# Kernel tuning notes

Hardware: AMD Instinct MI355X
Metric: run time of the kernel (lower is better)

The kernel has to match this reference:

```python
import jax, jax.numpy as jnp
import numpy as np

N = 50000      # nodes
E = 1600000    # edges (before self loops)
D = 128        # feature dim (input == hidden == final)
L = 3          # num_layers
EPS = 1e-5     # BatchNorm1d eps
SLOPE = 0.2    # GATConv leaky_relu negative slope


def setup_inputs() -> dict:
    key = jax.random.key(0)
    ks = jax.random.split(key, 5)
    x = jax.random.normal(ks[0], (N, D), jnp.float32)
    edge_index = jax.random.randint(ks[1], (2, E), 0, N)
    W = jax.random.normal(ks[2], (L, D, D), jnp.float32) * 0.1
    a_src = jax.random.normal(ks[3], (L, D), jnp.float32) * 0.1
    a_dst = jax.random.normal(ks[4], (L, D), jnp.float32) * 0.1
    b = jnp.zeros((L, D), jnp.float32)
    return {"x": x, "edge_index": edge_index, "W": W,
            "a_src": a_src, "a_dst": a_dst, "b": b}


def _gat_forward(x, src, dst, W, a_src, a_dst, b):
    z = x
    for l in range(L):
        h = z @ W[l]                                   # [N, D]
        # per-edge attention logits: alpha_src[j] + alpha_dst[i]
        e = jax.nn.leaky_relu((h @ a_src[l])[src] + (h @ a_dst[l])[dst], SLOPE)
        # segment softmax over incoming edges of each destination node
        m = jax.lax.stop_gradient(jax.ops.segment_max(e, dst, num_segments=N))
        p = jnp.exp(e - m[dst])
        s = jax.ops.segment_sum(p, dst, num_segments=N)
        alpha = p / s[dst]                             # [E+N]
        # scatter-aggregate weighted source features, add conv bias
        z = jax.ops.segment_sum(alpha[:, None] * h[src], dst, num_segments=N) + b[l]
        # fresh BatchNorm1d (training mode, weight=1, bias=0, biased var) -> ReLU
        mu = jnp.mean(z, axis=0)
        var = jnp.var(z, axis=0)
        z = jax.nn.relu((z - mu) * jax.lax.rsqrt(var + EPS))
        # dropout(p=0.5): identity in deterministic/eval reference
    return z


def reference(x, edge_index, W, a_src, a_dst, b):
    loops = jnp.arange(N, dtype=edge_index.dtype)
    src = jnp.concatenate([edge_index[0], loops])      # GATConv add_self_loops=True
    dst = jnp.concatenate([edge_index[1], loops])
    return _gat_forward(x, src, dst, W, a_src, a_dst, b)
```

## Files before the change

### kernel.cpp

```cpp
#include <hip/hip_runtime.h>
#include <hip/hip_bf16.h>
#include <math.h>

#define N_NODES 50000
#define N_EDGES 1600000
#define DIM 128
#define EPS 1e-5f
#define SLOPE 0.2f

#define NBUCK 256
#define NPB 196
#define EPB 4096
#define NBLK_B ((N_EDGES + EPB - 1) / EPB)

typedef __attribute__((ext_vector_type(8))) short bf16x8;
typedef __attribute__((ext_vector_type(4))) float f32x4;

__device__ __forceinline__ float lrelu(float x) { return x > 0.f ? x : SLOPE * x; }

__device__ __forceinline__ unsigned short f2bf(float f) {
    unsigned u = __float_as_uint(f);
    unsigned r = (u + 0x7fffu + ((u >> 16) & 1u)) >> 16;
    return (unsigned short)r;
}

__device__ __forceinline__ float2 ldh2(const unsigned short* p) {
    unsigned u = *(const unsigned*)p;
    float2 r;
    r.x = __uint_as_float(u << 16);
    r.y = __uint_as_float(u & 0xffff0000u);
    return r;
}

__global__ void k_hist(const int* __restrict__ dst, int* __restrict__ bcnt) {
    __shared__ int h[NBUCK];
    int tid = threadIdx.x;
    h[tid] = 0;
    __syncthreads();
    int nq = N_EDGES / 4;
    for (int q = blockIdx.x * 256 + tid; q < nq; q += gridDim.x * 256) {
        int4 d = ((const int4*)dst)[q];
        atomicAdd(&h[d.x / NPB], 1);
        atomicAdd(&h[d.y / NPB], 1);
        atomicAdd(&h[d.z / NPB], 1);
        atomicAdd(&h[d.w / NPB], 1);
    }
    __syncthreads();
    if (h[tid]) atomicAdd(&bcnt[tid], h[tid]);
}

__global__ void k_bscan(const int* __restrict__ bcnt, int* __restrict__ bbase,
                        int* __restrict__ gtail) {
    __shared__ int s[NBUCK];
    int t = threadIdx.x;
    int v = bcnt[t];
    s[t] = v;
    __syncthreads();
    for (int off = 1; off < NBUCK; off <<= 1) {
        int x = s[t];
        int y = (t >= off) ? s[t - off] : 0;
        __syncthreads();
        s[t] = x + y;
        __syncthreads();
    }
    bbase[t] = s[t] - v;
    gtail[t] = s[t] - v;
    if (t == NBUCK - 1) bbase[NBUCK] = s[NBUCK - 1];
}

__global__ __launch_bounds__(256) void k_partB(const int* __restrict__ src,
                                               const int* __restrict__ dst,
                                               int* __restrict__ gtail,
                                               uint2* __restrict__ staged) {
    __shared__ int cnt[NBUCK];
    __shared__ int bas[NBUCK];
    int tid = threadIdx.x;
    cnt[tid] = 0;
    __syncthreads();
    int e0 = blockIdx.x * EPB;
#pragma unroll 4
    for (int i = 0; i < EPB / 256; ++i) {
        int e = e0 + i * 256 + tid;
        if (e < N_EDGES) atomicAdd(&cnt[dst[e] / NPB], 1);
    }
    __syncthreads();
    {
        int c = cnt[tid];
        bas[tid] = c ? atomicAdd(&gtail[tid], c) : 0;
    }
    __syncthreads();
    cnt[tid] = 0;
    __syncthreads();
#pragma unroll 4
    for (int i = 0; i < EPB / 256; ++i) {
        int e = e0 + i * 256 + tid;
        if (e < N_EDGES) {
            int d = dst[e], s = src[e];
            int b = d / NPB;
            int off = atomicAdd(&cnt[b], 1);
            staged[bas[b] + off] = make_uint2((unsigned)s, (unsigned)d);
        }
    }
}

__global__ __launch_bounds__(256) void k_partC(const uint2* __restrict__ staged,
                                               const int* __restrict__ bbase,
                                               int* __restrict__ row_ptr,
                                               int* __restrict__ col_src) {
    __shared__ int cnt[NBUCK];
    __shared__ int loc[NBUCK];
    __shared__ int s[NBUCK];
    int b = blockIdx.x, tid = threadIdx.x;
    int d0 = b * NPB;
    int d1 = d0 + NPB;
    if (d1 > N_NODES) d1 = N_NODES;
    int nn = d1 - d0;
    int s0 = bbase[b], s1 = bbase[b + 1];

    cnt[tid] = 0;
    __syncthreads();
    for (int e = s0 + tid; e < s1; e += 256) {
        int d = (int)staged[e].y;
        atomicAdd(&cnt[d - d0], 1);
    }
    __syncthreads();
    {
        int v = cnt[tid];
        s[tid] = v;
        __syncthreads();
        for (int off = 1; off < NBUCK; off <<= 1) {
            int x = s[tid];
            int y = (tid >= off) ? s[tid - off] : 0;
            __syncthreads();
            s[tid] = x + y;
            __syncthreads();
        }
        loc[tid] = s[tid] - v;
    }
    if (tid < nn) row_ptr[d0 + tid] = s0 + loc[tid];
    if (b == 0 && tid == 0) row_ptr[N_NODES] = N_EDGES;
    cnt[tid] = 0;
    __syncthreads();
    for (int e = s0 + tid; e < s1; e += 256) {
        uint2 sd = staged[e];
        int d = (int)sd.y;
        int pos = s0 + loc[d - d0] + atomicAdd(&cnt[d - d0], 1);
        col_src[pos] = (int)sd.x;
    }
}

__global__ void k_prepW(const float* __restrict__ W, unsigned short* __restrict__ Wt) {
    int idx = blockIdx.x * 256 + threadIdx.x;
    int l = idx >> 14;
    int k = (idx >> 7) & 127;
    int c = idx & 127;
    Wt[l * 16384 + c * 128 + k] = f2bf(W[l * 16384 + k * 128 + c]);
}

__global__ __launch_bounds__(256) void k_gemm_mfma(const float* __restrict__ Z,
                                                   const unsigned short* __restrict__ Wt,
                                                   unsigned short* __restrict__ Hb,
                                                   const float* __restrict__ mu,
                                                   const float* __restrict__ rs,
                                                   const float* __restrict__ a_src,
                                                   const float* __restrict__ a_dst,
                                                   float* __restrict__ as_,
                                                   float* __restrict__ ad_) {
    __shared__ unsigned short Bs[128 * 128];
    int tid = threadIdx.x;
    int lane = tid & 63, wave = tid >> 6;

    {
        int c = tid >> 1, kh = tid & 1;
        const unsigned short* gsrc = &Wt[c * 128 + kh * 64];
#pragma unroll
        for (int ch = 0; ch < 8; ++ch) {
            int byte_off = (c * 256 + kh * 128 + ch * 16) ^ ((c & 7) << 4);
            *(int4*)((char*)Bs + byte_off) = *(const int4*)(gsrc + ch * 8);
        }
    }

    int r0 = blockIdx.x * 128 + wave * 32;
    bf16x8 afr[2][4];
#pragma unroll
    for (int rt = 0; rt < 2; ++rt) {
        int row = r0 + rt * 16 + (lane & 15);
        const float* zrow = &Z[(size_t)row * 128];
#pragma unroll
        for (int ks = 0; ks < 4; ++ks) {
            int k = ks * 32 + (lane >> 4) * 8;
            bf16x8 fr = (bf16x8){0, 0, 0, 0, 0, 0, 0, 0};
            if (row < N_NODES) {
                float4 a = *(const float4*)&zrow[k];
                float4 b = *(const float4*)&zrow[k + 4];
                if (mu) {
                    float4 m0 = *(const float4*)&mu[k];
                    float4 m1 = *(const float4*)&mu[k + 4];
                    float4 r0v = *(const float4*)&rs[k];
                    float4 r1v = *(const float4*)&rs[k + 4];
                    a.x = fmaxf((a.x - m0.x) * r0v.x, 0.f);
                    a.y = fmaxf((a.y - m0.y) * r0v.y, 0.f);
                    a.z = fmaxf((a.z - m0.z) * r0v.z, 0.f);
                    a.w = fmaxf((a.w - m0.w) * r0v.w, 0.f);
                    b.x = fmaxf((b.x - m1.x) * r1v.x, 0.f);
                    b.y = fmaxf((b.y - m1.y) * r1v.y, 0.f);
                    b.z = fmaxf((b.z - m1.z) * r1v.z, 0.f);
                    b.w = fmaxf((b.w - m1.w) * r1v.w, 0.f);
                }
                fr[0] = (short)f2bf(a.x); fr[1] = (short)f2bf(a.y);
                fr[2] = (short)f2bf(a.z); fr[3] = (short)f2bf(a.w);
                fr[4] = (short)f2bf(b.x); fr[5] = (short)f2bf(b.y);
                fr[6] = (short)f2bf(b.z); fr[7] = (short)f2bf(b.w);
            }
            afr[rt][ks] = fr;
        }
    }

    float asv[8], adv[8];
#pragma unroll
    for (int ct = 0; ct < 8; ++ct) {
        int c = ct * 16 + (lane & 15);
        asv[ct] = a_src[c];
        adv[ct] = a_dst[c];
    }
    __syncthreads();

    f32x4 acc[2][8];
#pragma unroll
    for (int rt = 0; rt < 2; ++rt)
#pragma unroll
        for (int ct = 0; ct < 8; ++ct) acc[rt][ct] = (f32x4){0.f, 0.f, 0.f, 0.f};

#pragma unroll
    for (int ct = 0; ct < 8; ++ct) {
        int c = ct * 16 + (lane & 15);
#pragma unroll
        for (int ks = 0; ks < 4; ++ks) {
            int k = ks * 32 + (lane >> 4) * 8;
            int byte_off = (c * 256 + k * 2) ^ ((c & 7) << 4);
            bf16x8 bfr = *(const bf16x8*)((char*)Bs + byte_off);
            acc[0][ct] = __builtin_amdgcn_mfma_f32_16x16x32_bf16(afr[0][ks], bfr, acc[0][ct], 0, 0, 0);
            acc[1][ct] = __builtin_amdgcn_mfma_f32_16x16x32_bf16(afr[1][ks], bfr, acc[1][ct], 0, 0, 0);
        }
    }

#pragma unroll
    for (int rt = 0; rt < 2; ++rt) {
#pragma unroll
        for (int ct = 0; ct < 8; ++ct) {
            int c = ct * 16 + (lane & 15);
#pragma unroll
            for (int j = 0; j < 4; ++j) {
                int row = r0 + rt * 16 + (lane >> 4) * 4 + j;
                if (row < N_NODES) Hb[(size_t)row * 128 + c] = f2bf(acc[rt][ct][j]);
            }
        }
#pragma unroll
        for (int j = 0; j < 4; ++j) {
            float ps = 0.f, pd = 0.f;
#pragma unroll
            for (int ct = 0; ct < 8; ++ct) {
                float v = acc[rt][ct][j];
                ps += v * asv[ct];
                pd += v * adv[ct];
            }
#pragma unroll
            for (int off = 8; off; off >>= 1) {
                ps += __shfl_xor(ps, off);
                pd += __shfl_xor(pd, off);
            }
            int row = r0 + rt * 16 + (lane >> 4) * 4 + j;
            if ((lane & 15) == 0 && row < N_NODES) {
                as_[row] = ps;
                ad_[row] = pd;
            }
        }
    }
}

__global__ void k_aggregate(const int* __restrict__ row_ptr, const int* __restrict__ col_src,
                            const unsigned short* __restrict__ Hb,
                            const float* __restrict__ as_, const float* __restrict__ ad_,
                            const float* __restrict__ bias, float* __restrict__ Zout,
                            float* __restrict__ ebuf) {
    int node = blockIdx.x * 4 + (threadIdx.x >> 6);
    int lane = threadIdx.x & 63;
    if (node >= N_NODES) return;

    int start = row_ptr[node], end = row_ptr[node + 1];
    int deg = end - start;
    float ad_i = ad_[node];
    float eself = lrelu(as_[node] + ad_i);
    float m = eself;
    float2 acc;
    float2 hi = ldh2(&Hb[(size_t)node * 128 + lane * 2]);

    if (deg <= 128) {
        int s0 = 0, s1 = 0;
        float e0 = -INFINITY, e1 = -INFINITY;
        if (start + lane < end) {
            s0 = col_src[start + lane];
            e0 = lrelu(as_[s0] + ad_i);
            m = fmaxf(m, e0);
        }
        if (start + 64 + lane < end) {
            s1 = col_src[start + 64 + lane];
            e1 = lrelu(as_[s1] + ad_i);
            m = fmaxf(m, e1);
        }
#pragma unroll
        for (int off = 32; off; off >>= 1) m = fmaxf(m, __shfl_xor(m, off));
        float w0 = __expf(e0 - m);
        float w1 = __expf(e1 - m);
        float p = w0 + w1;
#pragma unroll
        for (int off = 32; off; off >>= 1) p += __shfl_xor(p, off);
        float pself = __expf(eself - m);
        float inv_s = 1.f / (p + pself);
        w0 *= inv_s;
        w1 *= inv_s;
        float wself = pself * inv_s;
        acc.x = wself * hi.x;
        acc.y = wself * hi.y;

        int jmax = deg < 64 ? deg : 64;
        int j = 0;
        for (; j + 8 <= jmax; j += 8) {
            float w[8]; int sv[8];
#pragma unroll
            for (int q = 0; q < 8; ++q) {
                w[q] = __shfl(w0, j + q);
                sv[q] = __shfl(s0, j + q);
            }
            float2 h[8];
#pragma unroll
            for (int q = 0; q < 8; ++q) h[q] = ldh2(&Hb[(size_t)sv[q] * 128 + lane * 2]);
#pragma unroll
            for (int q = 0; q < 8; ++q) {
                acc.x += w[q] * h[q].x;
                acc.y += w[q] * h[q].y;
            }
        }
        for (; j < jmax; ++j) {
            float w = __shfl(w0, j);
            int sv = __shfl(s0, j);
            float2 hs = ldh2(&Hb[(size_t)sv * 128 + lane * 2]);
            acc.x += w * hs.x;
            acc.y += w * hs.y;
        }
        for (j = 64; j < deg; ++j) {
            float w = __shfl(w1, j - 64);
            int sv = __shfl(s1, j - 64);
            float2 hs = ldh2(&Hb[(size_t)sv * 128 + lane * 2]);
            acc.x += w * hs.x;
            acc.y += w * hs.y;
        }
    } else {
        for (int j = start + lane; j < end; j += 64) {
            int sj = col_src[j];
            float e = lrelu(as_[sj] + ad_i);
            ebuf[j] = e;
            m = fmaxf(m, e);
        }
#pragma unroll
        for (int off = 32; off; off >>= 1) m = fmaxf(m, __shfl_xor(m, off));
        float p = 0.f;
        for (int j = start + lane; j < end; j += 64) p += __expf(ebuf[j] - m);
#pragma unroll
        for (int off = 32; off; off >>= 1) p += __shfl_xor(p, off);
        float pself = __expf(eself - m);
        float inv_s = 1.f / (p + pself);
        float wself = pself * inv_s;
        acc.x = wself * hi.x;
        acc.y = wself * hi.y;
        for (int j = start; j < end; ++j) {
            int sv = col_src[j];
            float w = __expf(ebuf[j] - m) * inv_s;
            float2 hs = ldh2(&Hb[(size_t)sv * 128 + lane * 2]);
            acc.x += w * hs.x;
            acc.y += w * hs.y;
        }
    }

    float2 bv = *(const float2*)&bias[lane * 2];
    float2 o;
    o.x = acc.x + bv.x;
    o.y = acc.y + bv.y;
    *(float2*)&Zout[(size_t)node * 128 + lane * 2] = o;
}

__global__ void k_bnstats(const float* __restrict__ Z, float* __restrict__ part) {
    int c = threadIdx.x;
    float s = 0.f, sq = 0.f;
    for (int i = blockIdx.x; i < N_NODES; i += gridDim.x) {
        float v = Z[(size_t)i * 128 + c];
        s += v;
        sq += v * v;
    }
    part[blockIdx.x * 256 + c] = s;
    part[blockIdx.x * 256 + 128 + c] = sq;
}

__global__ void k_bnfinal(const float* __restrict__ part, float* __restrict__ mu,
                          float* __restrict__ rs) {
    int c = threadIdx.x;
    float s = 0.f, sq = 0.f;
    for (int b = 0; b < 512; ++b) {
        s += part[b * 256 + c];
        sq += part[b * 256 + 128 + c];
    }
    float m = s / (float)N_NODES;
    float var = sq / (float)N_NODES - m * m;
    mu[c] = m;
    rs[c] = rsqrtf(var + EPS);
}

__global__ void k_bnapply(const float* __restrict__ Zin, const float* __restrict__ mu,
                          const float* __restrict__ rs, float* __restrict__ Zout) {
    int idx = blockIdx.x * blockDim.x + threadIdx.x;
    if (idx >= N_NODES * 32) return;
    int c4 = idx & 31;
    float4 v = ((const float4*)Zin)[idx];
    float4 m4 = ((const float4*)mu)[c4];
    float4 r4 = ((const float4*)rs)[c4];
    v.x = fmaxf((v.x - m4.x) * r4.x, 0.f);
    v.y = fmaxf((v.y - m4.y) * r4.y, 0.f);
    v.z = fmaxf((v.z - m4.z) * r4.z, 0.f);
    v.w = fmaxf((v.w - m4.w) * r4.w, 0.f);
    ((float4*)Zout)[idx] = v;
}

extern "C" void kernel_launch(void* const* d_in, const int* in_sizes, int n_in,
                              void* d_out, int out_size, void* d_ws, size_t ws_size,
                              hipStream_t stream) {
    const float* x = (const float*)d_in[0];
    const int* ei = (const int*)d_in[1];
    const int* srcp = ei;
    const int* dstp = ei + N_EDGES;
    const float* W = (const float*)d_in[2];
    const float* a_src = (const float*)d_in[3];
    const float* a_dst = (const float*)d_in[4];
    const float* bias = (const float*)d_in[5];
    float* out = (float*)d_out;

    char* ws = (char*)d_ws;
    size_t off = 0;
    auto alloc = [&](size_t bytes) -> void* {
        void* p = ws + off;
        off = (off + bytes + 255) & ~(size_t)255;
        return p;
    };
    int* bcnt     = (int*)alloc(NBUCK * 4);
    int* bbase    = (int*)alloc((NBUCK + 1) * 4);
    int* gtail    = (int*)alloc(NBUCK * 4);
    int* row_ptr  = (int*)alloc((N_NODES + 1) * 4);
    int* col_src  = (int*)alloc(N_EDGES * 4);
    uint2* staged = (uint2*)alloc((size_t)N_EDGES * 8);
    unsigned short* hbf = (unsigned short*)alloc((size_t)N_NODES * DIM * 2);
    float* zbuf   = (float*)alloc((size_t)N_NODES * DIM * 4);
    unsigned short* wtb = (unsigned short*)alloc(3 * 16384 * 2);
    float* asb    = (float*)alloc(N_NODES * 4);
    float* adb    = (float*)alloc(N_NODES * 4);
    float* part   = (float*)alloc(512 * 256 * 4);
    float* mu     = (float*)alloc(128 * 4);
    float* rsg    = (float*)alloc(128 * 4);
    if (off > ws_size) return;

    float* ebuf = (float*)staged;

    hipMemsetAsync(bcnt, 0, NBUCK * 4, stream);
    k_hist<<<256, 256, 0, stream>>>(dstp, bcnt);
    k_bscan<<<1, NBUCK, 0, stream>>>(bcnt, bbase, gtail);
    k_partB<<<NBLK_B, 256, 0, stream>>>(srcp, dstp, gtail, staged);
    k_partC<<<NBUCK, 256, 0, stream>>>(staged, bbase, row_ptr, col_src);
    k_prepW<<<192, 256, 0, stream>>>(W, wtb);

    const float* zin = x;
    for (int l = 0; l < 3; ++l) {
        k_gemm_mfma<<<(N_NODES + 127) / 128, 256, 0, stream>>>(
            zin, wtb + l * 16384, hbf, (l == 0) ? nullptr : mu, rsg,
            a_src + l * DIM, a_dst + l * DIM, asb, adb);
        k_aggregate<<<(N_NODES + 3) / 4, 256, 0, stream>>>(row_ptr, col_src, hbf, asb, adb,
                                                           bias + l * DIM, zbuf, ebuf);
        k_bnstats<<<512, 128, 0, stream>>>(zbuf, part);
        k_bnfinal<<<1, 128, 0, stream>>>(part, mu, rsg);
        if (l == 2)
            k_bnapply<<<(N_NODES * 32 + 255) / 256, 256, 0, stream>>>(zbuf, mu, rsg, out);
        zin = zbuf;
    }
}
```

Before: 515.0 us.

## Split aggregation wave into four edge groups with 16-byte row loads

The aggregation kernel now assigns each quarter-wave of 16 lanes to a different neighbor edge. Each lane loads 8 bf16 features with a single 16-byte load instead of 2 features per lane. Partial sums are reduced across groups with cross-lane shuffles, and the self-loop term and bias are added in the final write. This widens memory transactions and puts four gathers in flight per iteration, at the cost of 8 accumulators per lane and extra shuffle reductions. Separately, the BN finalize kernel is widened from 128 to 512 threads, with a shared-memory reduction to shorten its serial loop.

```diff
diff --git a/kernel.cpp b/kernel.cpp
--- a/kernel.cpp
+++ b/kernel.cpp
@@ -26,6 +26,13 @@
 
 __device__ __forceinline__ float2 ldh2(const unsigned short* p) {
     unsigned u = *(const unsigned*)p;
+    float2 r;
+    r.x = __uint_as_float(u << 16);
+    r.y = __uint_as_float(u & 0xffff0000u);
+    return r;
+}
+
+__device__ __forceinline__ float2 bf2f2(unsigned u) {
     float2 r;
     r.x = __uint_as_float(u << 16);
     r.y = __uint_as_float(u & 0xffff0000u);
@@ -286,14 +293,18 @@
     int node = blockIdx.x * 4 + (threadIdx.x >> 6);
     int lane = threadIdx.x & 63;
     if (node >= N_NODES) return;
+    int g = lane >> 4;
+    int fl = lane & 15;
 
     int start = row_ptr[node], end = row_ptr[node + 1];
     int deg = end - start;
     float ad_i = ad_[node];
     float eself = lrelu(as_[node] + ad_i);
     float m = eself;
-    float2 acc;
-    float2 hi = ldh2(&Hb[(size_t)node * 128 + lane * 2]);
+    float acc[8];
+#pragma unroll
+    for (int f = 0; f < 8; ++f) acc[f] = 0.f;
+    float wself;
 
     if (deg <= 128) {
         int s0 = 0, s1 = 0;
@@ -319,41 +330,30 @@
         float inv_s = 1.f / (p + pself);
         w0 *= inv_s;
         w1 *= inv_s;
-        float wself = pself * inv_s;
-        acc.x = wself * hi.x;
-        acc.y = wself * hi.y;
+        wself = pself * inv_s;
 
         int jmax = deg < 64 ? deg : 64;
-        int j = 0;
-        for (; j + 8 <= jmax; j += 8) {
-            float w[8]; int sv[8];
-#pragma unroll
-            for (int q = 0; q < 8; ++q) {
-                w[q] = __shfl(w0, j + q);
-                sv[q] = __shfl(s0, j + q);
-            }
-            float2 h[8];
-#pragma unroll
-            for (int q = 0; q < 8; ++q) h[q] = ldh2(&Hb[(size_t)sv[q] * 128 + lane * 2]);
-#pragma unroll
-            for (int q = 0; q < 8; ++q) {
-                acc.x += w[q] * h[q].x;
-                acc.y += w[q] * h[q].y;
-            }
-        }
-        for (; j < jmax; ++j) {
-            float w = __shfl(w0, j);
-            int sv = __shfl(s0, j);
-            float2 hs = ldh2(&Hb[(size_t)sv * 128 + lane * 2]);
-            acc.x += w * hs.x;
-            acc.y += w * hs.y;
-        }
-        for (j = 64; j < deg; ++j) {
-            float w = __shfl(w1, j - 64);
-            int sv = __shfl(s1, j - 64);
-            float2 hs = ldh2(&Hb[(size_t)sv * 128 + lane * 2]);
-            acc.x += w * hs.x;
-            acc.y += w * hs.y;
+        for (int j = 0; j < jmax; j += 4) {
+            int idx = j + g;
+            float w = __shfl(w0, idx);
+            int sv = __shfl(s0, idx);
+            uint4 hv = *(const uint4*)&Hb[(size_t)sv * 128 + fl * 8];
+            float2 a0 = bf2f2(hv.x), a1 = bf2f2(hv.y), a2 = bf2f2(hv.z), a3 = bf2f2(hv.w);
+            acc[0] += w * a0.x; acc[1] += w * a0.y;
+            acc[2] += w * a1.x; acc[3] += w * a1.y;
+            acc[4] += w * a2.x; acc[5] += w * a2.y;
+            acc[6] += w * a3.x; acc[7] += w * a3.y;
+        }
+        for (int j = 64; j < deg; j += 4) {
+            int idx = j - 64 + g;
+            float w = __shfl(w1, idx);
+            int sv = __shfl(s1, idx);
+            uint4 hv = *(const uint4*)&Hb[(size_t)sv * 128 + fl * 8];
+            float2 a0 = bf2f2(hv.x), a1 = bf2f2(hv.y), a2 = bf2f2(hv.z), a3 = bf2f2(hv.w);
+            acc[0] += w * a0.x; acc[1] += w * a0.y;
+            acc[2] += w * a1.x; acc[3] += w * a1.y;
+            acc[4] += w * a2.x; acc[5] += w * a2.y;
+            acc[6] += w * a3.x; acc[7] += w * a3.y;
         }
     } else {
         for (int j = start + lane; j < end; j += 64) {
@@ -370,23 +370,47 @@
         for (int off = 32; off; off >>= 1) p += __shfl_xor(p, off);
         float pself = __expf(eself - m);
         float inv_s = 1.f / (p + pself);
-        float wself = pself * inv_s;
-        acc.x = wself * hi.x;
-        acc.y = wself * hi.y;
-        for (int j = start; j < end; ++j) {
-            int sv = col_src[j];
-            float w = __expf(ebuf[j] - m) * inv_s;
-            float2 hs = ldh2(&Hb[(size_t)sv * 128 + lane * 2]);
-            acc.x += w * hs.x;
-            acc.y += w * hs.y;
-        }
-    }
-
-    float2 bv = *(const float2*)&bias[lane * 2];
-    float2 o;
-    o.x = acc.x + bv.x;
-    o.y = acc.y + bv.y;
-    *(float2*)&Zout[(size_t)node * 128 + lane * 2] = o;
+        wself = pself * inv_s;
+        for (int j = start; j < end; j += 4) {
+            int e = j + g;
+            float w = 0.f;
+            int sv = 0;
+            if (e < end) {
+                w = __expf(ebuf[e] - m) * inv_s;
+                sv = col_src[e];
+            }
+            uint4 hv = *(const uint4*)&Hb[(size_t)sv * 128 + fl * 8];
+            float2 a0 = bf2f2(hv.x), a1 = bf2f2(hv.y), a2 = bf2f2(hv.z), a3 = bf2f2(hv.w);
+            acc[0] += w * a0.x; acc[1] += w * a0.y;
+            acc[2] += w * a1.x; acc[3] += w * a1.y;
+            acc[4] += w * a2.x; acc[5] += w * a2.y;
+            acc[6] += w * a3.x; acc[7] += w * a3.y;
+        }
+    }
+
+#pragma unroll
+    for (int f = 0; f < 8; ++f) {
+        acc[f] += __shfl_xor(acc[f], 16);
+        acc[f] += __shfl_xor(acc[f], 32);
+    }
+
+    if (g == 0) {
+        uint4 hv = *(const uint4*)&Hb[(size_t)node * 128 + fl * 8];
+        float2 a0 = bf2f2(hv.x), a1 = bf2f2(hv.y), a2 = bf2f2(hv.z), a3 = bf2f2(hv.w);
+        float4 b0 = *(const float4*)&bias[fl * 8];
+        float4 b1 = *(const float4*)&bias[fl * 8 + 4];
+        float4 o0, o1;
+        o0.x = acc[0] + wself * a0.x + b0.x;
+        o0.y = acc[1] + wself * a0.y + b0.y;
+        o0.z = acc[2] + wself * a1.x + b0.z;
+        o0.w = acc[3] + wself * a1.y + b0.w;
+        o1.x = acc[4] + wself * a2.x + b1.x;
+        o1.y = acc[5] + wself * a2.y + b1.y;
+        o1.z = acc[6] + wself * a3.x + b1.z;
+        o1.w = acc[7] + wself * a3.y + b1.w;
+        *(float4*)&Zout[(size_t)node * 128 + fl * 8] = o0;
+        *(float4*)&Zout[(size_t)node * 128 + fl * 8 + 4] = o1;
+    }
 }
 
 __global__ void k_bnstats(const float* __restrict__ Z, float* __restrict__ part) {
@@ -403,16 +427,26 @@
 
 __global__ void k_bnfinal(const float* __restrict__ part, float* __restrict__ mu,
                           float* __restrict__ rs) {
-    int c = threadIdx.x;
+    __shared__ float ss[4][128];
+    __shared__ float sqq[4][128];
+    int c = threadIdx.x & 127;
+    int q = threadIdx.x >> 7;
     float s = 0.f, sq = 0.f;
-    for (int b = 0; b < 512; ++b) {
+    for (int b = q; b < 512; b += 4) {
         s += part[b * 256 + c];
         sq += part[b * 256 + 128 + c];
     }
-    float m = s / (float)N_NODES;
-    float var = sq / (float)N_NODES - m * m;
-    mu[c] = m;
-    rs[c] = rsqrtf(var + EPS);
+    ss[q][c] = s;
+    sqq[q][c] = sq;
+    __syncthreads();
+    if (q == 0) {
+        s = ss[0][c] + ss[1][c] + ss[2][c] + ss[3][c];
+        sq = sqq[0][c] + sqq[1][c] + sqq[2][c] + sqq[3][c];
+        float m = s / (float)N_NODES;
+        float var = sq / (float)N_NODES - m * m;
+        mu[c] = m;
+        rs[c] = rsqrtf(var + EPS);
+    }
 }
 
 __global__ void k_bnapply(const float* __restrict__ Zin, const float* __restrict__ mu,
@@ -483,7 +517,7 @@
         k_aggregate<<<(N_NODES + 3) / 4, 256, 0, stream>>>(row_ptr, col_src, hbf, asb, adb,
                                                            bias + l * DIM, zbuf, ebuf);
         k_bnstats<<<512, 128, 0, stream>>>(zbuf, part);
-        k_bnfinal<<<1, 128, 0, stream>>>(part, mu, rsg);
+        k_bnfinal<<<1, 512, 0, stream>>>(part, mu, rsg);
         if (l == 2)
             k_bnapply<<<(N_NODES * 32 + 255) / 256, 256, 0, stream>>>(zbuf, mu, rsg, out);
         zin = zbuf;
```

After: 557.9 us. +8.3%, slower.
